# Optimization experiments

Hardware: AMD Instinct MI355X
Metric: run time of the kernel (lower is better)

## Reference

```python
import jax, jax.numpy as jnp
import numpy as np

NUM_EXPERTS = 8


def setup_inputs() -> dict:
    key = jax.random.key(0)
    k1, k2, k3, k4 = jax.random.split(key, 4)
    T, H, I, E = 1024, 1024, 4096, NUM_EXPERTS
    return {
        "hidden_states": jax.random.normal(k1, (T, H), dtype=jnp.float32),
        "w1": jax.random.normal(k2, (E, 2 * I, H), dtype=jnp.float32) * 0.02,
        "w2": jax.random.normal(k3, (E, H, I), dtype=jnp.float32) * 0.02,
        "gating_output": jax.random.normal(k4, (T, E), dtype=jnp.float32),
        "topk": 2,
    }


def reference(hidden_states, w1, w2, gating_output, topk):
    # Faithful single-device version of jax_fused_moe_func (renormalize=True,
    # reduce_results=True). The original sorts token copies by expert id and runs
    # a grouped matmul (megablox gmm), then reverts the sort; mathematically each
    # token copy is multiplied by its expert's weights, which we compute directly
    # (no sort/unsort permutation needed since it cancels).
    orig_shape = hidden_states.shape
    dtype = hidden_states.dtype
    H = hidden_states.shape[-1]
    T = hidden_states.size // H
    E = w1.shape[0]
    I = w2.shape[-1]  # intermediate_size

    hs = hidden_states.reshape(T, H)
    gates = gating_output.reshape(T, E)

    probs = jax.nn.softmax(gates.astype(jnp.float32), axis=-1)
    topk_weights, topk_indices = jax.lax.top_k(probs, k=topk)
    topk_weights = topk_weights / topk_weights.sum(axis=-1, keepdims=True)  # renormalize
    topk_weights = topk_weights.astype(dtype)

    flat_ids = topk_indices.reshape(-1)            # [T*topk] expert id per token copy
    x = jnp.repeat(hs, topk, axis=0)               # [T*topk, H] token copies

    out = jnp.zeros((T * topk, H), dtype=dtype)
    for e in range(E):  # fixed small expert loop (emulates grouped GEMM)
        h = x @ w1[e].T                            # [m, 2I]
        act = jax.nn.silu(h[:, :I]) * h[:, I:]     # SwiGLU
        y = act @ w2[e].T                          # [m, H]
        out = jnp.where((flat_ids == e)[:, None], y, out)

    out = (out.reshape(T, topk, H) * topk_weights[..., None]).sum(axis=-2)
    return out.reshape(orig_shape)
```

## Files before the change

### kernel.cpp

```cpp
#include <hip/hip_runtime.h>

#define T_TOK 1024
#define H_DIM 1024
#define I_DIM 4096
#define NE 8

typedef __attribute__((ext_vector_type(8))) short bf16x8;
typedef __attribute__((ext_vector_type(4))) float f32x4;
typedef __attribute__((ext_vector_type(8))) unsigned short us8;

__device__ __forceinline__ unsigned short f2bf(float x) {
  union { float f; unsigned u; } v; v.f = x;
  unsigned r = v.u + 0x7fffu + ((v.u >> 16) & 1u);
  return (unsigned short)(r >> 16);
}

__device__ __forceinline__ unsigned cvt_pk_bf16(float a, float b) {
  unsigned r;
  asm("v_cvt_pk_bf16_f32 %0, %1, %2" : "=v"(r) : "v"(a), "v"(b));
  return r;
}

__global__ void k_route(const float* __restrict__ gates, int* __restrict__ counts,
                        int* __restrict__ tok_idx, float* __restrict__ tok_w,
                        int* __restrict__ tok_cpy) {
  int t = blockIdx.x * blockDim.x + threadIdx.x;
  if (t >= T_TOK) return;
  float g[NE];
#pragma unroll
  for (int e = 0; e < NE; ++e) g[e] = gates[t * NE + e];
  int i1 = 0; float g1 = g[0];
#pragma unroll
  for (int e = 1; e < NE; ++e) if (g[e] > g1) { g1 = g[e]; i1 = e; }
  int i2 = -1; float g2 = -1e30f;
#pragma unroll
  for (int e = 0; e < NE; ++e) if (e != i1 && g[e] > g2) { g2 = g[e]; i2 = e; }
  float wa = 1.0f / (1.0f + expf(g2 - g1));
  float wb = 1.0f - wa;
  int s1 = atomicAdd(&counts[i1], 1);
  tok_idx[i1 * T_TOK + s1] = t; tok_w[i1 * T_TOK + s1] = wa; tok_cpy[i1 * T_TOK + s1] = 0;
  int s2 = atomicAdd(&counts[i2], 1);
  tok_idx[i2 * T_TOK + s2] = t; tok_w[i2 * T_TOK + s2] = wb; tok_cpy[i2 * T_TOK + s2] = 1;
}

__global__ void k_pack(const float* __restrict__ hs, const int* __restrict__ counts,
                       const int* __restrict__ tok_idx, const float* __restrict__ tok_w,
                       const int* __restrict__ tok_cpy, unsigned short* __restrict__ xpack,
                       float* __restrict__ row_w, int* __restrict__ inv_row) {
  int e = blockIdx.x >> 10, slot = blockIdx.x & 1023;
  if (slot >= counts[e]) return;
  int off = 0;
#pragma unroll
  for (int i = 0; i < NE; ++i) if (i < e) off += counts[i];
  int row = off + slot;
  int tok = tok_idx[e * T_TOK + slot];
  if (threadIdx.x == 0) {
    row_w[row] = tok_w[e * T_TOK + slot];
    inv_row[tok * 2 + tok_cpy[e * T_TOK + slot]] = row;
  }
  float4 v = ((const float4*)(hs + (size_t)tok * H_DIM))[threadIdx.x];
  uint2 o; o.x = cvt_pk_bf16(v.x, v.y); o.y = cvt_pk_bf16(v.z, v.w);
  ((uint2*)(xpack + (size_t)row * H_DIM))[threadIdx.x] = o;
}

#define BK 64

__global__ __launch_bounds__(256)
void k_gemm1(const float* __restrict__ w1, const unsigned short* __restrict__ xpack,
             const int* __restrict__ counts, unsigned short* __restrict__ act) {
  int b = blockIdx.x;
  int x = b & 7, s = b >> 3;
  int mt = s & 7, pl = s >> 3;
  int panel = pl * 8 + x;
  int e = panel >> 7, ntile = panel & 127;
  int cnt = counts[e];
  int m0 = mt * 128;
  if (m0 >= cnt) return;
  int off = 0;
#pragma unroll
  for (int i = 0; i < NE; ++i) if (i < e) off += counts[i];
  int n0 = ntile * 32;

  __shared__ __align__(16) short As[128 * BK];
  __shared__ __align__(16) short Bs[64 * BK];

  int tid = threadIdx.x;
  int lane = tid & 63, wid = tid >> 6;
  int wm = wid & 1, wn = wid >> 1;
  int lr = lane & 15, lk8 = (lane >> 4) * 8;

  const float* w1e = w1 + (size_t)e * (2 * I_DIM) * H_DIM;
  const unsigned short* xb = xpack + (size_t)(off + m0) * H_DIM;

  int arow0 = tid >> 3, ack = tid & 7;
  int brow0 = tid >> 4, bck = tid & 15;

  const unsigned short* aptr[4];
  int awoff[4];
#pragma unroll
  for (int i = 0; i < 4; ++i) {
    int r = arow0 + i * 32;
    aptr[i] = xb + (size_t)r * H_DIM + ack * 8;
    awoff[i] = r * BK + ((ack * 8) ^ ((r & 7) << 3));
  }
  const float* bptr[4];
  int bwoff[4];
#pragma unroll
  for (int i = 0; i < 4; ++i) {
    int r = brow0 + i * 16;
    int grow = ((r & 16) ? I_DIM : 0) + n0 + ((r >> 5) << 4) + (r & 15);
    bptr[i] = w1e + (size_t)grow * H_DIM + bck * 4;
    bwoff[i] = r * BK + ((bck * 4) ^ ((r & 7) << 3));
  }

  f32x4 acc[4][2];
#pragma unroll
  for (int i = 0; i < 4; ++i)
#pragma unroll
    for (int j = 0; j < 2; ++j) acc[i][j] = (f32x4){0.f, 0.f, 0.f, 0.f};

  us8 aReg[4];
  float4 bReg[4];

  auto loadA = [&](int k0) {
#pragma unroll
    for (int i = 0; i < 4; ++i) {
      us8 z = {0, 0, 0, 0, 0, 0, 0, 0};
      aReg[i] = (m0 + arow0 + i * 32 < cnt) ? *(const us8*)(aptr[i] + k0) : z;
    }
  };
  auto loadB = [&](int k0) {
#pragma unroll
    for (int i = 0; i < 4; ++i) bReg[i] = *(const float4*)(bptr[i] + k0);
  };

  loadA(0); loadB(0);

  for (int ks = 0; ks < H_DIM / BK; ++ks) {
    __syncthreads();
#pragma unroll
    for (int i = 0; i < 4; ++i) *(us8*)&As[awoff[i]] = aReg[i];
#pragma unroll
    for (int i = 0; i < 4; ++i) {
      float4 v = bReg[i];
      uint2 o; o.x = cvt_pk_bf16(v.x, v.y); o.y = cvt_pk_bf16(v.z, v.w);
      *(uint2*)&Bs[bwoff[i]] = o;
    }
    __syncthreads();
    if (ks + 1 < H_DIM / BK) { loadA((ks + 1) * BK); loadB((ks + 1) * BK); }
#pragma unroll
    for (int kk = 0; kk < 2; ++kk) {
      int k0 = kk * 32 + lk8;
      bf16x8 a[4], bb[2];
#pragma unroll
      for (int mr = 0; mr < 4; ++mr) {
        int r = wm * 64 + mr * 16 + lr;
        a[mr] = *(const bf16x8*)&As[r * BK + (k0 ^ ((r & 7) << 3))];
      }
#pragma unroll
      for (int nr = 0; nr < 2; ++nr) {
        int r = (wn * 2 + nr) * 16 + lr;
        bb[nr] = *(const bf16x8*)&Bs[r * BK + (k0 ^ ((r & 7) << 3))];
      }
#pragma unroll
      for (int mr = 0; mr < 4; ++mr)
#pragma unroll
        for (int nr = 0; nr < 2; ++nr)
          acc[mr][nr] = __builtin_amdgcn_mfma_f32_16x16x32_bf16(a[mr], bb[nr], acc[mr][nr], 0, 0, 0);
    }
  }

#pragma unroll
  for (int mr = 0; mr < 4; ++mr) {
    f32x4 g = acc[mr][0], u = acc[mr][1];
    int ncol = n0 + wn * 16 + lr;
#pragma unroll
    for (int q = 0; q < 4; ++q) {
      int rl = wm * 64 + mr * 16 + (lane >> 4) * 4 + q;
      if (m0 + rl < cnt) {
        float gv = g[q];
        float av = gv / (1.0f + expf(-gv)) * u[q];
        act[(size_t)(off + m0 + rl) * I_DIM + ncol] = f2bf(av);
      }
    }
  }
}

__global__ __launch_bounds__(256)
void k_gemm2(const float* __restrict__ w2, const unsigned short* __restrict__ act,
             const int* __restrict__ counts, const float* __restrict__ row_w,
             float* __restrict__ yp) {
  int b = blockIdx.x;
  int x = b & 7, s = b >> 3;
  int mt = s & 15, pl = s >> 4;
  int panel = pl * 8 + x;
  int e = panel >> 6;
  int nt = (panel & 63) >> 2, kc = panel & 3;
  int cnt = counts[e];
  int m0 = mt * 64;
  if (m0 >= cnt) return;
  int off = 0;
#pragma unroll
  for (int i = 0; i < NE; ++i) if (i < e) off += counts[i];
  int n0 = nt * 64;
  int kbase = kc * 1024;

  __shared__ __align__(16) short As[64 * BK];
  __shared__ __align__(16) short Bs[64 * BK];

  int tid = threadIdx.x;
  int lane = tid & 63, wid = tid >> 6;
  int wm = wid & 1, wn = wid >> 1;
  int lr = lane & 15, lk8 = (lane >> 4) * 8;

  const float* w2e = w2 + (size_t)e * H_DIM * I_DIM;
  const unsigned short* ab = act + (size_t)(off + m0) * I_DIM;

  int arow0 = tid >> 3, ack = tid & 7;
  int brow0 = tid >> 4, bck = tid & 15;

  const unsigned short* aptr[2];
  int awoff[2];
#pragma unroll
  for (int i = 0; i < 2; ++i) {
    int r = arow0 + i * 32;
    aptr[i] = ab + (size_t)r * I_DIM + kbase + ack * 8;
    awoff[i] = r * BK + ((ack * 8) ^ ((r & 7) << 3));
  }
  const float* bptr[4];
  int bwoff[4];
#pragma unroll
  for (int i = 0; i < 4; ++i) {
    int r = brow0 + i * 16;
    bptr[i] = w2e + (size_t)(n0 + r) * I_DIM + kbase + bck * 4;
    bwoff[i] = r * BK + ((bck * 4) ^ ((r & 7) << 3));
  }

  f32x4 acc[2][2];
#pragma unroll
  for (int i = 0; i < 2; ++i)
#pragma unroll
    for (int j = 0; j < 2; ++j) acc[i][j] = (f32x4){0.f, 0.f, 0.f, 0.f};

  us8 aReg[2];
  float4 bReg[4];

  auto loadA = [&](int k0) {
#pragma unroll
    for (int i = 0; i < 2; ++i) {
      us8 z = {0, 0, 0, 0, 0, 0, 0, 0};
      aReg[i] = (m0 + arow0 + i * 32 < cnt) ? *(const us8*)(aptr[i] + k0) : z;
    }
  };
  auto loadB = [&](int k0) {
#pragma unroll
    for (int i = 0; i < 4; ++i) bReg[i] = *(const float4*)(bptr[i] + k0);
  };

  loadA(0); loadB(0);

  for (int ks = 0; ks < 1024 / BK; ++ks) {
    __syncthreads();
#pragma unroll
    for (int i = 0; i < 2; ++i) *(us8*)&As[awoff[i]] = aReg[i];
#pragma unroll
    for (int i = 0; i < 4; ++i) {
      float4 v = bReg[i];
      uint2 o; o.x = cvt_pk_bf16(v.x, v.y); o.y = cvt_pk_bf16(v.z, v.w);
      *(uint2*)&Bs[bwoff[i]] = o;
    }
    __syncthreads();
    if (ks + 1 < 1024 / BK) { loadA((ks + 1) * BK); loadB((ks + 1) * BK); }
#pragma unroll
    for (int kk = 0; kk < 2; ++kk) {
      int k0 = kk * 32 + lk8;
      bf16x8 a[2], bb[2];
#pragma unroll
      for (int mr = 0; mr < 2; ++mr) {
        int r = wm * 32 + mr * 16 + lr;
        a[mr] = *(const bf16x8*)&As[r * BK + (k0 ^ ((r & 7) << 3))];
      }
#pragma unroll
      for (int nr = 0; nr < 2; ++nr) {
        int r = wn * 32 + nr * 16 + lr;
        bb[nr] = *(const bf16x8*)&Bs[r * BK + (k0 ^ ((r & 7) << 3))];
      }
#pragma unroll
      for (int mr = 0; mr < 2; ++mr)
#pragma unroll
        for (int nr = 0; nr < 2; ++nr)
          acc[mr][nr] = __builtin_amdgcn_mfma_f32_16x16x32_bf16(a[mr], bb[nr], acc[mr][nr], 0, 0, 0);
    }
  }

  float* ypc = yp + (size_t)kc * (2048 * H_DIM);
#pragma unroll
  for (int mr = 0; mr < 2; ++mr) {
#pragma unroll
    for (int q = 0; q < 4; ++q) {
      int rl = wm * 32 + mr * 16 + (lane >> 4) * 4 + q;
      if (m0 + rl >= cnt) continue;
      int grow = off + m0 + rl;
      float wgt = row_w[grow];
      float* yrow = ypc + (size_t)grow * H_DIM;
#pragma unroll
      for (int nr = 0; nr < 2; ++nr) {
        int ncol = n0 + wn * 32 + nr * 16 + lr;
        yrow[ncol] = acc[mr][nr][q] * wgt;
      }
    }
  }
}

__global__ void k_combine(const float* __restrict__ yp, const int* __restrict__ inv_row,
                          float* __restrict__ out) {
  int t = blockIdx.x, i = threadIdx.x;
  int r0 = inv_row[2 * t], r1 = inv_row[2 * t + 1];
  float4 s = make_float4(0.f, 0.f, 0.f, 0.f);
#pragma unroll
  for (int kc = 0; kc < 4; ++kc) {
    const float4* a = (const float4*)(yp + (size_t)kc * (2048 * H_DIM) + (size_t)r0 * H_DIM);
    const float4* b = (const float4*)(yp + (size_t)kc * (2048 * H_DIM) + (size_t)r1 * H_DIM);
    float4 va = a[i], vb = b[i];
    s.x += va.x + vb.x; s.y += va.y + vb.y; s.z += va.z + vb.z; s.w += va.w + vb.w;
  }
  ((float4*)(out + (size_t)t * H_DIM))[i] = s;
}

extern "C" void kernel_launch(void* const* d_in, const int* in_sizes, int n_in,
                              void* d_out, int out_size, void* d_ws, size_t ws_size,
                              hipStream_t stream) {
  const float* hs = (const float*)d_in[0];
  const float* w1 = (const float*)d_in[1];
  const float* w2 = (const float*)d_in[2];
  const float* gates = (const float*)d_in[3];
  float* out = (float*)d_out;

  char* ws = (char*)d_ws;
  int* counts = (int*)ws;
  int* tok_idx = (int*)(ws + 4096);
  float* tok_w = (float*)(ws + 4096 + 32768);
  int* tok_cpy = (int*)(ws + 4096 + 65536);
  float* row_w = (float*)(ws + 4096 + 98304);
  int* inv_row = (int*)(ws + 4096 + 98304 + 8192);
  unsigned short* xpack = (unsigned short*)(ws + (1 << 17));
  unsigned short* act = (unsigned short*)(ws + (8u << 20));
  float* yp = (float*)(ws + (32u << 20));

  hipMemsetAsync(counts, 0, NE * sizeof(int), stream);
  k_route<<<dim3(4), dim3(256), 0, stream>>>(gates, counts, tok_idx, tok_w, tok_cpy);
  k_pack<<<dim3(NE * T_TOK), dim3(256), 0, stream>>>(hs, counts, tok_idx, tok_w, tok_cpy,
                                                     xpack, row_w, inv_row);
  k_gemm1<<<dim3(8192), dim3(256), 0, stream>>>(w1, xpack, counts, act);
  k_gemm2<<<dim3(8192), dim3(256), 0, stream>>>(w2, act, counts, row_w, yp);
  k_combine<<<dim3(T_TOK), dim3(256), 0, stream>>>(yp, inv_row, out);
}
```

Measured before the change: 222.1 us.

## Double-buffer LDS and register prefetch in both expert GEMMs, reorder block mapping

Both GEMM kernels now use two LDS buffers and two register prefetch sets. That drops one of the two barriers per K step and issues global loads two steps ahead of use, to hide fp32 weight load latency. The block-to-tile mapping also changes: blocks now iterate panels first, then M tiles, which alters L2 reuse of the weight panels across M tiles. The cost is doubled LDS use and more registers per block, which may lower occupancy.

Result: slower. 245.0 us (+10.3%).

```diff
diff --git a/kernel.cpp b/kernel.cpp
--- a/kernel.cpp
+++ b/kernel.cpp
@@ -19,6 +19,11 @@
   unsigned r;
   asm("v_cvt_pk_bf16_f32 %0, %1, %2" : "=v"(r) : "v"(a), "v"(b));
   return r;
+}
+
+__device__ __forceinline__ void sync_lds() {
+  asm volatile("s_waitcnt lgkmcnt(0)" ::: "memory");
+  __builtin_amdgcn_s_barrier();
 }
 
 __global__ void k_route(const float* __restrict__ gates, int* __restrict__ counts,
@@ -69,9 +74,8 @@
 void k_gemm1(const float* __restrict__ w1, const unsigned short* __restrict__ xpack,
              const int* __restrict__ counts, unsigned short* __restrict__ act) {
   int b = blockIdx.x;
-  int x = b & 7, s = b >> 3;
-  int mt = s & 7, pl = s >> 3;
-  int panel = pl * 8 + x;
+  int panel = b & 1023;
+  int mt = b >> 10;
   int e = panel >> 7, ntile = panel & 127;
   int cnt = counts[e];
   int m0 = mt * 128;
@@ -81,8 +85,8 @@
   for (int i = 0; i < NE; ++i) if (i < e) off += counts[i];
   int n0 = ntile * 32;
 
-  __shared__ __align__(16) short As[128 * BK];
-  __shared__ __align__(16) short Bs[64 * BK];
+  __shared__ __align__(16) short As[2][128 * BK];
+  __shared__ __align__(16) short Bs[2][64 * BK];
 
   int tid = threadIdx.x;
   int lane = tid & 63, wid = tid >> 6;
@@ -119,56 +123,57 @@
 #pragma unroll
     for (int j = 0; j < 2; ++j) acc[i][j] = (f32x4){0.f, 0.f, 0.f, 0.f};
 
-  us8 aReg[4];
-  float4 bReg[4];
-
-  auto loadA = [&](int k0) {
-#pragma unroll
-    for (int i = 0; i < 4; ++i) {
-      us8 z = {0, 0, 0, 0, 0, 0, 0, 0};
-      aReg[i] = (m0 + arow0 + i * 32 < cnt) ? *(const us8*)(aptr[i] + k0) : z;
-    }
-  };
-  auto loadB = [&](int k0) {
-#pragma unroll
-    for (int i = 0; i < 4; ++i) bReg[i] = *(const float4*)(bptr[i] + k0);
-  };
-
-  loadA(0); loadB(0);
-
-  for (int ks = 0; ks < H_DIM / BK; ++ks) {
-    __syncthreads();
-#pragma unroll
-    for (int i = 0; i < 4; ++i) *(us8*)&As[awoff[i]] = aReg[i];
-#pragma unroll
-    for (int i = 0; i < 4; ++i) {
-      float4 v = bReg[i];
-      uint2 o; o.x = cvt_pk_bf16(v.x, v.y); o.y = cvt_pk_bf16(v.z, v.w);
-      *(uint2*)&Bs[bwoff[i]] = o;
-    }
-    __syncthreads();
-    if (ks + 1 < H_DIM / BK) { loadA((ks + 1) * BK); loadB((ks + 1) * BK); }
-#pragma unroll
-    for (int kk = 0; kk < 2; ++kk) {
-      int k0 = kk * 32 + lk8;
-      bf16x8 a[4], bb[2];
-#pragma unroll
-      for (int mr = 0; mr < 4; ++mr) {
-        int r = wm * 64 + mr * 16 + lr;
-        a[mr] = *(const bf16x8*)&As[r * BK + (k0 ^ ((r & 7) << 3))];
-      }
-#pragma unroll
-      for (int nr = 0; nr < 2; ++nr) {
-        int r = (wn * 2 + nr) * 16 + lr;
-        bb[nr] = *(const bf16x8*)&Bs[r * BK + (k0 ^ ((r & 7) << 3))];
-      }
-#pragma unroll
-      for (int mr = 0; mr < 4; ++mr)
-#pragma unroll
-        for (int nr = 0; nr < 2; ++nr)
-          acc[mr][nr] = __builtin_amdgcn_mfma_f32_16x16x32_bf16(a[mr], bb[nr], acc[mr][nr], 0, 0, 0);
-    }
-  }
+  us8 aReg[2][4];
+  float4 bReg[2][4];
+
+#define G1_LOAD(SET, KSTEP)                                                     \
+  {                                                                             \
+    int kq = (KSTEP)*BK;                                                        \
+    _Pragma("unroll") for (int i = 0; i < 4; ++i) {                             \
+      us8 z = {0, 0, 0, 0, 0, 0, 0, 0};                                         \
+      aReg[SET][i] = (m0 + arow0 + i * 32 < cnt) ? *(const us8*)(aptr[i] + kq) : z; \
+    }                                                                           \
+    _Pragma("unroll") for (int i = 0; i < 4; ++i)                               \
+        bReg[SET][i] = *(const float4*)(bptr[i] + kq);                          \
+  }
+
+#define G1_STEP(BUF, SET, NEXTK)                                                \
+  {                                                                             \
+    _Pragma("unroll") for (int i = 0; i < 4; ++i)                               \
+        *(us8*)&As[BUF][awoff[i]] = aReg[SET][i];                               \
+    _Pragma("unroll") for (int i = 0; i < 4; ++i) {                             \
+      float4 v = bReg[SET][i];                                                  \
+      uint2 o; o.x = cvt_pk_bf16(v.x, v.y); o.y = cvt_pk_bf16(v.z, v.w);        \
+      *(uint2*)&Bs[BUF][bwoff[i]] = o;                                          \
+    }                                                                           \
+    if ((NEXTK) < H_DIM / BK) G1_LOAD(SET, NEXTK);                              \
+    sync_lds();                                                                 \
+    _Pragma("unroll") for (int kk = 0; kk < 2; ++kk) {                          \
+      int k0 = kk * 32 + lk8;                                                   \
+      bf16x8 a[4], bb[2];                                                       \
+      _Pragma("unroll") for (int mr = 0; mr < 4; ++mr) {                        \
+        int r = wm * 64 + mr * 16 + lr;                                         \
+        a[mr] = *(const bf16x8*)&As[BUF][r * BK + (k0 ^ ((r & 7) << 3))];       \
+      }                                                                         \
+      _Pragma("unroll") for (int nr = 0; nr < 2; ++nr) {                        \
+        int r = (wn * 2 + nr) * 16 + lr;                                        \
+        bb[nr] = *(const bf16x8*)&Bs[BUF][r * BK + (k0 ^ ((r & 7) << 3))];      \
+      }                                                                         \
+      _Pragma("unroll") for (int mr = 0; mr < 4; ++mr)                          \
+          _Pragma("unroll") for (int nr = 0; nr < 2; ++nr)                      \
+              acc[mr][nr] = __builtin_amdgcn_mfma_f32_16x16x32_bf16(            \
+                  a[mr], bb[nr], acc[mr][nr], 0, 0, 0);                         \
+    }                                                                           \
+  }
+
+  G1_LOAD(0, 0);
+  G1_LOAD(1, 1);
+  for (int ks = 0; ks < H_DIM / BK; ks += 2) {
+    G1_STEP(0, 0, ks + 2);
+    G1_STEP(1, 1, ks + 3);
+  }
+#undef G1_LOAD
+#undef G1_STEP
 
 #pragma unroll
   for (int mr = 0; mr < 4; ++mr) {
@@ -191,9 +196,8 @@
              const int* __restrict__ counts, const float* __restrict__ row_w,
              float* __restrict__ yp) {
   int b = blockIdx.x;
-  int x = b & 7, s = b >> 3;
-  int mt = s & 15, pl = s >> 4;
-  int panel = pl * 8 + x;
+  int panel = b & 511;
+  int mt = b >> 9;
   int e = panel >> 6;
   int nt = (panel & 63) >> 2, kc = panel & 3;
   int cnt = counts[e];
@@ -205,8 +209,8 @@
   int n0 = nt * 64;
   int kbase = kc * 1024;
 
-  __shared__ __align__(16) short As[64 * BK];
-  __shared__ __align__(16) short Bs[64 * BK];
+  __shared__ __align__(16) short As[2][64 * BK];
+  __shared__ __align__(16) short Bs[2][64 * BK];
 
   int tid = threadIdx.x;
   int lane = tid & 63, wid = tid >> 6;
@@ -242,56 +246,57 @@
 #pragma unroll
     for (int j = 0; j < 2; ++j) acc[i][j] = (f32x4){0.f, 0.f, 0.f, 0.f};
 
-  us8 aReg[2];
-  float4 bReg[4];
-
-  auto loadA = [&](int k0) {
-#pragma unroll
-    for (int i = 0; i < 2; ++i) {
-      us8 z = {0, 0, 0, 0, 0, 0, 0, 0};
-      aReg[i] = (m0 + arow0 + i * 32 < cnt) ? *(const us8*)(aptr[i] + k0) : z;
-    }
-  };
-  auto loadB = [&](int k0) {
-#pragma unroll
-    for (int i = 0; i < 4; ++i) bReg[i] = *(const float4*)(bptr[i] + k0);
-  };
-
-  loadA(0); loadB(0);
-
-  for (int ks = 0; ks < 1024 / BK; ++ks) {
-    __syncthreads();
-#pragma unroll
-    for (int i = 0; i < 2; ++i) *(us8*)&As[awoff[i]] = aReg[i];
-#pragma unroll
-    for (int i = 0; i < 4; ++i) {
-      float4 v = bReg[i];
-      uint2 o; o.x = cvt_pk_bf16(v.x, v.y); o.y = cvt_pk_bf16(v.z, v.w);
-      *(uint2*)&Bs[bwoff[i]] = o;
-    }
-    __syncthreads();
-    if (ks + 1 < 1024 / BK) { loadA((ks + 1) * BK); loadB((ks + 1) * BK); }
-#pragma unroll
-    for (int kk = 0; kk < 2; ++kk) {
-      int k0 = kk * 32 + lk8;
-      bf16x8 a[2], bb[2];
-#pragma unroll
-      for (int mr = 0; mr < 2; ++mr) {
-        int r = wm * 32 + mr * 16 + lr;
-        a[mr] = *(const bf16x8*)&As[r * BK + (k0 ^ ((r & 7) << 3))];
-      }
-#pragma unroll
-      for (int nr = 0; nr < 2; ++nr) {
-        int r = wn * 32 + nr * 16 + lr;
-        bb[nr] = *(const bf16x8*)&Bs[r * BK + (k0 ^ ((r & 7) << 3))];
-      }
-#pragma unroll
-      for (int mr = 0; mr < 2; ++mr)
-#pragma unroll
-        for (int nr = 0; nr < 2; ++nr)
-          acc[mr][nr] = __builtin_amdgcn_mfma_f32_16x16x32_bf16(a[mr], bb[nr], acc[mr][nr], 0, 0, 0);
-    }
-  }
+  us8 aReg[2][2];
+  float4 bReg[2][4];
+
+#define G2_LOAD(SET, KSTEP)                                                     \
+  {                                                                             \
+    int kq = (KSTEP)*BK;                                                        \
+    _Pragma("unroll") for (int i = 0; i < 2; ++i) {                             \
+      us8 z = {0, 0, 0, 0, 0, 0, 0, 0};                                         \
+      aReg[SET][i] = (m0 + arow0 + i * 32 < cnt) ? *(const us8*)(aptr[i] + kq) : z; \
+    }                                                                           \
+    _Pragma("unroll") for (int i = 0; i < 4; ++i)                               \
+        bReg[SET][i] = *(const float4*)(bptr[i] + kq);                          \
+  }
+
+#define G2_STEP(BUF, SET, NEXTK)                                                \
+  {                                                                             \
+    _Pragma("unroll") for (int i = 0; i < 2; ++i)                               \
+        *(us8*)&As[BUF][awoff[i]] = aReg[SET][i];                               \
+    _Pragma("unroll") for (int i = 0; i < 4; ++i) {                             \
+      float4 v = bReg[SET][i];                                                  \
+      uint2 o; o.x = cvt_pk_bf16(v.x, v.y); o.y = cvt_pk_bf16(v.z, v.w);        \
+      *(uint2*)&Bs[BUF][bwoff[i]] = o;                                          \
+    }                                                                           \
+    if ((NEXTK) < 16) G2_LOAD(SET, NEXTK);                                      \
+    sync_lds();                                                                 \
+    _Pragma("unroll") for (int kk = 0; kk < 2; ++kk) {                          \
+      int k0 = kk * 32 + lk8;                                                   \
+      bf16x8 a[2], bb[2];                                                       \
+      _Pragma("unroll") for (int mr = 0; mr < 2; ++mr) {                        \
+        int r = wm * 32 + mr * 16 + lr;                                         \
+        a[mr] = *(const bf16x8*)&As[BUF][r * BK + (k0 ^ ((r & 7) << 3))];       \
+      }                                                                         \
+      _Pragma("unroll") for (int nr = 0; nr < 2; ++nr) {                        \
+        int r = wn * 32 + nr * 16 + lr;                                         \
+        bb[nr] = *(const bf16x8*)&Bs[BUF][r * BK + (k0 ^ ((r & 7) << 3))];      \
+      }                                                                         \
+      _Pragma("unroll") for (int mr = 0; mr < 2; ++mr)                          \
+          _Pragma("unroll") for (int nr = 0; nr < 2; ++nr)                      \
+              acc[mr][nr] = __builtin_amdgcn_mfma_f32_16x16x32_bf16(            \
+                  a[mr], bb[nr], acc[mr][nr], 0, 0, 0);                         \
+    }                                                                           \
+  }
+
+  G2_LOAD(0, 0);
+  G2_LOAD(1, 1);
+  for (int ks = 0; ks < 16; ks += 2) {
+    G2_STEP(0, 0, ks + 2);
+    G2_STEP(1, 1, ks + 3);
+  }
+#undef G2_LOAD
+#undef G2_STEP
 
   float* ypc = yp + (size_t)kc * (2048 * H_DIM);
 #pragma unroll
```
